# Kernel optimization log

Measured on AMD Instinct MI355X. Metric: run time of the kernel, lower is better.

## Reference

```python
import jax, jax.numpy as jnp
import numpy as np

N_NODES = 100000
N_EDGES = 1600000
DIM = 128
HEADS = 8
PHC = DIM // HEADS  # per-head channels = 16


def setup_inputs() -> dict:
    key = jax.random.key(0)
    k1, k2, k3, k4, k5 = jax.random.split(key, 5)
    nodes = jax.random.normal(k1, (N_NODES, DIM), dtype=jnp.float32)
    senders = jax.random.randint(k2, (N_EDGES,), 0, N_NODES, dtype=jnp.int32)
    receivers = jax.random.randint(k3, (N_EDGES,), 0, N_NODES, dtype=jnp.int32)
    # VarianceScaling(fan_avg, uniform) ~ limit = sqrt(3/fan_avg)
    lim_w = np.sqrt(3.0 / DIM)
    W = jax.random.uniform(k4, (DIM, DIM), minval=-lim_w, maxval=lim_w, dtype=jnp.float32)
    b = jnp.zeros((DIM,), dtype=jnp.float32)
    lim_a = np.sqrt(3.0 * 2.0 / (2 * PHC + 1))
    attn_w = jax.random.uniform(k5, (2 * PHC, 1), minval=-lim_a, maxval=lim_a, dtype=jnp.float32)
    attn_b = jnp.zeros((1,), dtype=jnp.float32)
    return {"nodes": nodes, "senders": senders, "receivers": receivers,
            "W": W, "b": b, "attn_w": attn_w, "attn_b": attn_b}


def reference(nodes, senders, receivers, W, b, attn_w, attn_b):
    n = nodes.shape[0]
    # linear transform + split heads: [N, H, PHC]
    nt = (nodes @ W + b).reshape(n, HEADS, PHC)
    sent = nt[senders]      # [E, H, PHC] gather
    recv = nt[receivers]    # [E, H, PHC] gather
    # attention logits: Linear(1) over leaky_relu(concat(q,k)) -> [E, H, 1]
    qk = jax.nn.leaky_relu(jnp.concatenate([sent, recv], axis=-1), negative_slope=0.2)
    logits = qk @ attn_w + attn_b  # [E, H, 1]
    # segment softmax over edges grouped by receiver node
    seg_max = jax.ops.segment_max(logits, receivers, num_segments=n)  # [N, H, 1]
    exp = jnp.exp(logits - seg_max[receivers])
    denom = jax.ops.segment_sum(exp, receivers, num_segments=n)  # [N, H, 1]
    alpha = exp / denom[receivers]
    # weighted scatter-sum of sender features
    out = jax.ops.segment_sum(sent * alpha, receivers, num_segments=n)  # [N, H, PHC]
    return out.reshape(n, -1)  # concat=True -> [N, DIM]
```

## Files before the change

### kernel.cpp

```cpp
#include <hip/hip_runtime.h>

#define DIM 128
#define HEADS 8
#define PHC 16

#define BSHIFT 6
#define BNODES 64
#define CAP 1408
#define NBMAX 1600

typedef __bf16 bf16x4 __attribute__((ext_vector_type(4)));
typedef __bf16 bf16x8 __attribute__((ext_vector_type(8)));
typedef float  f32x4  __attribute__((ext_vector_type(4)));

__device__ inline unsigned short f2bf(float x) {
  unsigned int u = __float_as_uint(x);
  unsigned int r = (u + 0x7FFF + ((u >> 16) & 1)) >> 16;
  return (unsigned short)r;
}

#define GROWS 64

__global__ __launch_bounds__(256, 3) void k_gemm(
    const float* __restrict__ A, const float* __restrict__ W,
    const float* __restrict__ bias, const float* __restrict__ attn_w,
    unsigned int* __restrict__ nt_bf, float* __restrict__ s_exp,
    int* __restrict__ gCursor, int NB, int n) {
  __shared__ __align__(16) float smemF[GROWS * DIM];
  __bf16* Ah = (__bf16*)smemF;
  __bf16* Al = Ah + GROWS * DIM;
  const int t    = threadIdx.x;
  const int row0 = blockIdx.x * GROWS;
  const int lane = t & 63;
  const int w    = t >> 6;
  const int lg   = lane >> 4;
  const int ln   = lane & 15;

  if (blockIdx.x == 0)
    for (int i = t; i < NB; i += 256) gCursor[i] = 0;

  float4 av[8];
  {
    const float4* A4 = (const float4*)(A + (size_t)row0 * DIM);
    const int lim = min(GROWS, n - row0) * (DIM / 4);
#pragma unroll
    for (int j = 0; j < 8; ++j) {
      int i = t + j * 256;
      av[j] = (i < lim) ? A4[i] : make_float4(0.f, 0.f, 0.f, 0.f);
    }
  }

  bf16x8 Bh[4][2], Bl[4][2];
  {
    const int wc = (w << 5) + ln;
#pragma unroll
    for (int kt = 0; kt < 4; ++kt)
#pragma unroll
      for (int ct = 0; ct < 2; ++ct)
#pragma unroll
        for (int e = 0; e < 8; ++e) {
          int k = (kt << 5) + ((e >> 2) << 4) + (lg << 2) + (e & 3);
          float wv = W[k * DIM + wc + (ct << 4)];
          __bf16 h = (__bf16)wv;
          Bh[kt][ct][e] = h;
          Bl[kt][ct][e] = (__bf16)(wv - (float)h);
        }
  }

#pragma unroll
  for (int j = 0; j < 8; ++j) {
    int i = t + j * 256;
    int r = i >> 5, c4 = i & 31;
    int ei = (r << 7) + ((c4 << 2) ^ ((r & 7) << 3));
    float x0 = av[j].x, x1 = av[j].y, x2 = av[j].z, x3 = av[j].w;
    __bf16 h0 = (__bf16)x0, h1 = (__bf16)x1, h2 = (__bf16)x2, h3 = (__bf16)x3;
    bf16x4 hv = {h0, h1, h2, h3};
    bf16x4 lv = {(__bf16)(x0 - (float)h0), (__bf16)(x1 - (float)h1),
                 (__bf16)(x2 - (float)h2), (__bf16)(x3 - (float)h3)};
    *(bf16x4*)(Ah + ei) = hv;
    *(bf16x4*)(Al + ei) = lv;
  }

  f32x4 acc[4][2];
  {
    const float b0 = bias[(w << 5) + ln];
    const float b1 = bias[(w << 5) + 16 + ln];
#pragma unroll
    for (int rt = 0; rt < 4; ++rt) {
      acc[rt][0] = (f32x4){b0, b0, b0, b0};
      acc[rt][1] = (f32x4){b1, b1, b1, b1};
    }
  }
  __syncthreads();

#pragma unroll
  for (int kt = 0; kt < 4; ++kt) {
    bf16x8 ah[4], al[4];
#pragma unroll
    for (int rt = 0; rt < 4; ++rt) {
      int m    = (rt << 4) + ln;
      int base = m << 7;
      int sw   = (m & 7) << 3;
      int k0   = (kt << 5) + (lg << 2);
      bf16x4 u0 = *(const bf16x4*)(Ah + base + (k0 ^ sw));
      bf16x4 u1 = *(const bf16x4*)(Ah + base + ((k0 + 16) ^ sw));
      bf16x4 v0 = *(const bf16x4*)(Al + base + (k0 ^ sw));
      bf16x4 v1 = *(const bf16x4*)(Al + base + ((k0 + 16) ^ sw));
      ah[rt] = __builtin_shufflevector(u0, u1, 0, 1, 2, 3, 4, 5, 6, 7);
      al[rt] = __builtin_shufflevector(v0, v1, 0, 1, 2, 3, 4, 5, 6, 7);
    }
#pragma unroll
    for (int rt = 0; rt < 4; ++rt)
#pragma unroll
      for (int ct = 0; ct < 2; ++ct) {
        acc[rt][ct] = __builtin_amdgcn_mfma_f32_16x16x32_bf16(
            ah[rt], Bh[kt][ct], acc[rt][ct], 0, 0, 0);
        acc[rt][ct] = __builtin_amdgcn_mfma_f32_16x16x32_bf16(
            ah[rt], Bl[kt][ct], acc[rt][ct], 0, 0, 0);
        acc[rt][ct] = __builtin_amdgcn_mfma_f32_16x16x32_bf16(
            al[rt], Bh[kt][ct], acc[rt][ct], 0, 0, 0);
      }
  }

  __syncthreads();

#pragma unroll
  for (int rt = 0; rt < 4; ++rt)
#pragma unroll
    for (int ct = 0; ct < 2; ++ct) {
      int colx = ((w << 5) + (ct << 4) + ln) ^ ((lg & 1) << 4);
#pragma unroll
      for (int r = 0; r < 4; ++r) {
        int rowl = (rt << 4) + (lg << 2) + r;
        smemF[(rowl << 7) + colx] = acc[rt][ct][r];
      }
    }

  {
    const float aw = attn_w[ln];
#pragma unroll
    for (int rt = 0; rt < 4; ++rt)
#pragma unroll
      for (int ct = 0; ct < 2; ++ct) {
        const int head = (w << 1) + ct;
#pragma unroll
        for (int r = 0; r < 4; ++r) {
          float v = acc[rt][ct][r];
          float p = (v > 0.f ? v : 0.2f * v) * aw;
          p += __shfl_xor(p, 1);
          p += __shfl_xor(p, 2);
          p += __shfl_xor(p, 4);
          p += __shfl_xor(p, 8);
          if (ln == 0) {
            int row = row0 + (rt << 4) + (lg << 2) + r;
            if (row < n) s_exp[row * HEADS + head] = __expf(p);
          }
        }
      }
  }
  __syncthreads();

  {
    const int nrow = min(GROWS, n - row0);
#pragma unroll
    for (int j = 0; j < 8; ++j) {
      int i = t + j * 256;
      int r = i >> 5, c4 = i & 31;
      if (r < nrow) {
        int c4s = c4 ^ (((r >> 2) & 1) << 2);
        f32x4 v = *(const f32x4*)(smemF + (r << 7) + (c4s << 2));
        unsigned int lo = (unsigned int)f2bf(v[0]) | ((unsigned int)f2bf(v[1]) << 16);
        unsigned int hi = (unsigned int)f2bf(v[2]) | ((unsigned int)f2bf(v[3]) << 16);
        ((uint2*)nt_bf)[(size_t)(row0 + r) * 32 + c4] = make_uint2(lo, hi);
      }
    }
  }
}

__global__ __launch_bounds__(256) void k_scatterpairs(
    const int* __restrict__ send, const int* __restrict__ recv,
    int* __restrict__ gCursor, unsigned int* __restrict__ pairs,
    int E, int NB) {
  __shared__ int cnt[NBMAX];
  __shared__ int cur[NBMAX];
  const int t = threadIdx.x;
  for (int i = t; i < NB; i += 256) cnt[i] = 0;
  __syncthreads();
  const int e0 = blockIdx.x * 8192;
  const int e1 = min(e0 + 8192, E);
  for (int i = e0 + t; i < e1; i += 256)
    atomicAdd(&cnt[recv[i] >> BSHIFT], 1);
  __syncthreads();
  for (int i = t; i < NB; i += 256) {
    int c = cnt[i];
    cur[i] = i * CAP + (c ? atomicAdd(&gCursor[i], c) : 0);
  }
  __syncthreads();
  for (int i = e0 + t; i < e1; i += 256) {
    int r = recv[i];
    int b = r >> BSHIFT;
    int p = atomicAdd(&cur[b], 1);
    if (p - b * CAP < CAP)
      pairs[p] = (unsigned int)send[i] | ((unsigned int)(r & (BNODES - 1)) << 17);
  }
}

__global__ __launch_bounds__(256) void k_aggbuild(
    const unsigned int* __restrict__ pairs, const int* __restrict__ gCursor,
    const unsigned int* __restrict__ nt_bf, const float* __restrict__ s_exp,
    float* __restrict__ out, int n) {
  __shared__ unsigned int buf[CAP];
  __shared__ int csr_l[CAP];
  __shared__ int hist[BNODES], offl[BNODES], curl[BNODES];
  const int b = blockIdx.x;
  const int t = threadIdx.x;
  const int base = b * CAP;
  const int bsize = min(gCursor[b], CAP);

  for (int i = t; i < bsize; i += 256) buf[i] = pairs[base + i];
  if (t < BNODES) hist[t] = 0;
  __syncthreads();
  for (int i = t; i < bsize; i += 256)
    atomicAdd(&hist[(buf[i] >> 17) & (BNODES - 1)], 1);
  __syncthreads();
  if (t < 64) {
    int v = hist[t];
    int x = v;
#pragma unroll
    for (int off = 1; off < 64; off <<= 1) {
      int y = __shfl_up(x, off);
      if (t >= off) x += y;
    }
    offl[t] = x - v;
    curl[t] = x - v;
  }
  __syncthreads();
  for (int i = t; i < bsize; i += 256) {
    unsigned int v = buf[i];
    int p = atomicAdd(&curl[(v >> 17) & (BNODES - 1)], 1);
    csr_l[p] = (int)(v & 0x1FFFF);
  }
  __syncthreads();

  const int wv = t >> 6;
  const int lane = t & 63;
  const int half = lane >> 5;
  const int l32 = lane & 31;
  const int head = l32 >> 2;
  const uint2* nt2 = (const uint2*)nt_bf;

#pragma unroll 1
  for (int pi = 0; pi < 8; ++pi) {
    const int nl = wv * 16 + pi * 2 + half;
    const int node = (b << BSHIFT) + nl;
    const int deg = hist[nl];
    const int eoff = offl[nl];
    float4 acc = make_float4(0.f, 0.f, 0.f, 0.f);
    float den = 0.f;
    for (int j = 0; j < deg; j += 2) {
      int s0 = csr_l[eoff + j];
      bool ok1 = (j + 1) < deg;
      int s1 = csr_l[ok1 ? (eoff + j + 1) : eoff];
      float w0 = s_exp[s0 * HEADS + head];
      float w1 = ok1 ? s_exp[s1 * HEADS + head] : 0.f;
      uint2 q0 = nt2[(size_t)s0 * 32 + l32];
      uint2 q1 = nt2[(size_t)s1 * 32 + l32];
      den += w0 + w1;
      acc.x = fmaf(w0, __uint_as_float(q0.x << 16),
              fmaf(w1, __uint_as_float(q1.x << 16), acc.x));
      acc.y = fmaf(w0, __uint_as_float(q0.x & 0xFFFF0000u),
              fmaf(w1, __uint_as_float(q1.x & 0xFFFF0000u), acc.y));
      acc.z = fmaf(w0, __uint_as_float(q0.y << 16),
              fmaf(w1, __uint_as_float(q1.y << 16), acc.z));
      acc.w = fmaf(w0, __uint_as_float(q0.y & 0xFFFF0000u),
              fmaf(w1, __uint_as_float(q1.y & 0xFFFF0000u), acc.w));
    }
    if (node < n) {
      const float inv = (deg > 0) ? 1.0f / den : 0.f;
      ((float4*)out)[(size_t)node * 32 + l32] =
          make_float4(acc.x * inv, acc.y * inv, acc.z * inv, acc.w * inv);
    }
  }
}

extern "C" void kernel_launch(void* const* d_in, const int* in_sizes, int n_in,
                              void* d_out, int out_size, void* d_ws, size_t ws_size,
                              hipStream_t stream) {
  const float* nodes   = (const float*)d_in[0];
  const int*   senders = (const int*)d_in[1];
  const int*   recvs   = (const int*)d_in[2];
  const float* W       = (const float*)d_in[3];
  const float* bias    = (const float*)d_in[4];
  const float* attn_w  = (const float*)d_in[5];

  const int n = in_sizes[0] / DIM;
  const int E = in_sizes[1];
  const int NB = (n + BNODES - 1) >> BSHIFT;

  char* w = (char*)d_ws;
  auto align256 = [](size_t x) { return (x + 255) & ~(size_t)255; };
  size_t off = 0;
  unsigned int* nt_bf = (unsigned int*)(w + off); off += align256((size_t)n * DIM * 2);
  float* s_exp   = (float*)(w + off); off += align256((size_t)n * HEADS * 4);
  unsigned int* pairs = (unsigned int*)(w + off); off += align256((size_t)NB * CAP * 4);
  int* gCursor   = (int*)(w + off);   off += align256((size_t)NB * 4);
  (void)ws_size;

  k_gemm<<<(n + GROWS - 1) / GROWS, 256, 0, stream>>>(nodes, W, bias, attn_w,
                                                      nt_bf, s_exp, gCursor, NB, n);
  const int nb1 = (E + 8191) / 8192;
  k_scatterpairs<<<nb1, 256, 0, stream>>>(senders, recvs, gCursor, pairs, E, NB);
  k_aggbuild<<<NB, 256, 0, stream>>>(pairs, gCursor, nt_bf, s_exp,
                                     (float*)d_out, n);
}
```

Before: 274.7 us.

## Pre-split W into bf16 hi/lo fragments, widen LDS reads and aggregation loads

Adds a small kernel that converts W into MFMA-ready bf16 hi/lo fragment arrays once, so each GEMM block loads fragments per k-tile with vector loads instead of gathering and splitting 128 scalars per thread. This also lowers register pressure. The A tile in LDS is re-swizzled at 16-byte units so each fragment is a single bf16x8 read. The aggregation kernel now processes four nodes per wave with 16 lanes each, using 16-byte loads and a 4-way unrolled edge loop to get more memory-level parallelism, at the cost of one extra launch and more live registers.

Measured after the change: 268.2 us. 1.02x faster.

```diff
diff --git a/kernel.cpp b/kernel.cpp
--- a/kernel.cpp
+++ b/kernel.cpp
@@ -19,13 +19,35 @@
   return (unsigned short)r;
 }
 
+__global__ __launch_bounds__(256) void k_prepw(
+    const float* __restrict__ W, __bf16* __restrict__ Wh,
+    __bf16* __restrict__ Wl) {
+  const int tuple = blockIdx.x * 256 + threadIdx.x;
+  const int ln = tuple & 15;
+  const int lg = (tuple >> 4) & 3;
+  const int cg = (tuple >> 6) & 7;
+  const int kt = tuple >> 9;
+  const int col = (cg << 4) + ln;
+  bf16x8 h, l;
+#pragma unroll
+  for (int e = 0; e < 8; ++e) {
+    int k = (kt << 5) + ((e >> 2) << 4) + (lg << 2) + (e & 3);
+    float wv = W[k * DIM + col];
+    __bf16 hh = (__bf16)wv;
+    h[e] = hh;
+    l[e] = (__bf16)(wv - (float)hh);
+  }
+  *(bf16x8*)(Wh + tuple * 8) = h;
+  *(bf16x8*)(Wl + tuple * 8) = l;
+}
+
 #define GROWS 64
 
 __global__ __launch_bounds__(256, 3) void k_gemm(
-    const float* __restrict__ A, const float* __restrict__ W,
-    const float* __restrict__ bias, const float* __restrict__ attn_w,
-    unsigned int* __restrict__ nt_bf, float* __restrict__ s_exp,
-    int* __restrict__ gCursor, int NB, int n) {
+    const float* __restrict__ A, const __bf16* __restrict__ Wh,
+    const __bf16* __restrict__ Wl, const float* __restrict__ bias,
+    const float* __restrict__ attn_w, unsigned int* __restrict__ nt_bf,
+    float* __restrict__ s_exp, int* __restrict__ gCursor, int NB, int n) {
   __shared__ __align__(16) float smemF[GROWS * DIM];
   __bf16* Ah = (__bf16*)smemF;
   __bf16* Al = Ah + GROWS * DIM;
@@ -50,28 +72,13 @@
     }
   }
 
-  bf16x8 Bh[4][2], Bl[4][2];
-  {
-    const int wc = (w << 5) + ln;
-#pragma unroll
-    for (int kt = 0; kt < 4; ++kt)
-#pragma unroll
-      for (int ct = 0; ct < 2; ++ct)
-#pragma unroll
-        for (int e = 0; e < 8; ++e) {
-          int k = (kt << 5) + ((e >> 2) << 4) + (lg << 2) + (e & 3);
-          float wv = W[k * DIM + wc + (ct << 4)];
-          __bf16 h = (__bf16)wv;
-          Bh[kt][ct][e] = h;
-          Bl[kt][ct][e] = (__bf16)(wv - (float)h);
-        }
-  }
-
 #pragma unroll
   for (int j = 0; j < 8; ++j) {
     int i = t + j * 256;
     int r = i >> 5, c4 = i & 31;
-    int ei = (r << 7) + ((c4 << 2) ^ ((r & 7) << 3));
+    int ktc = c4 >> 3, lgc = c4 & 3, ehi = (c4 >> 2) & 1;
+    int unit = (r << 4) + (((ktc << 2) + lgc) ^ (r & 15));
+    int ei = (unit << 3) + (ehi << 2);
     float x0 = av[j].x, x1 = av[j].y, x2 = av[j].z, x3 = av[j].w;
     __bf16 h0 = (__bf16)x0, h1 = (__bf16)x1, h2 = (__bf16)x2, h3 = (__bf16)x3;
     bf16x4 hv = {h0, h1, h2, h3};
@@ -93,33 +100,35 @@
   }
   __syncthreads();
 
+  const int cg0 = w << 1;
 #pragma unroll
   for (int kt = 0; kt < 4; ++kt) {
+    bf16x8 Bh0, Bl0, Bh1, Bl1;
+    {
+      int i0 = ((((kt << 3) + cg0) << 2) + lg) * 16 + ln;
+      int i1 = ((((kt << 3) + cg0 + 1) << 2) + lg) * 16 + ln;
+      Bh0 = *(const bf16x8*)(Wh + (i0 << 3));
+      Bl0 = *(const bf16x8*)(Wl + (i0 << 3));
+      Bh1 = *(const bf16x8*)(Wh + (i1 << 3));
+      Bl1 = *(const bf16x8*)(Wl + (i1 << 3));
+    }
     bf16x8 ah[4], al[4];
 #pragma unroll
     for (int rt = 0; rt < 4; ++rt) {
-      int m    = (rt << 4) + ln;
-      int base = m << 7;
-      int sw   = (m & 7) << 3;
-      int k0   = (kt << 5) + (lg << 2);
-      bf16x4 u0 = *(const bf16x4*)(Ah + base + (k0 ^ sw));
-      bf16x4 u1 = *(const bf16x4*)(Ah + base + ((k0 + 16) ^ sw));
-      bf16x4 v0 = *(const bf16x4*)(Al + base + (k0 ^ sw));
-      bf16x4 v1 = *(const bf16x4*)(Al + base + ((k0 + 16) ^ sw));
-      ah[rt] = __builtin_shufflevector(u0, u1, 0, 1, 2, 3, 4, 5, 6, 7);
-      al[rt] = __builtin_shufflevector(v0, v1, 0, 1, 2, 3, 4, 5, 6, 7);
-    }
-#pragma unroll
-    for (int rt = 0; rt < 4; ++rt)
-#pragma unroll
-      for (int ct = 0; ct < 2; ++ct) {
-        acc[rt][ct] = __builtin_amdgcn_mfma_f32_16x16x32_bf16(
-            ah[rt], Bh[kt][ct], acc[rt][ct], 0, 0, 0);
-        acc[rt][ct] = __builtin_amdgcn_mfma_f32_16x16x32_bf16(
-            ah[rt], Bl[kt][ct], acc[rt][ct], 0, 0, 0);
-        acc[rt][ct] = __builtin_amdgcn_mfma_f32_16x16x32_bf16(
-            al[rt], Bh[kt][ct], acc[rt][ct], 0, 0, 0);
-      }
+      int m = (rt << 4) + ln;
+      int u = (m << 4) + (((kt << 2) + lg) ^ (m & 15));
+      ah[rt] = *(const bf16x8*)(Ah + (u << 3));
+      al[rt] = *(const bf16x8*)(Al + (u << 3));
+    }
+#pragma unroll
+    for (int rt = 0; rt < 4; ++rt) {
+      acc[rt][0] = __builtin_amdgcn_mfma_f32_16x16x32_bf16(ah[rt], Bh0, acc[rt][0], 0, 0, 0);
+      acc[rt][0] = __builtin_amdgcn_mfma_f32_16x16x32_bf16(ah[rt], Bl0, acc[rt][0], 0, 0, 0);
+      acc[rt][0] = __builtin_amdgcn_mfma_f32_16x16x32_bf16(al[rt], Bh0, acc[rt][0], 0, 0, 0);
+      acc[rt][1] = __builtin_amdgcn_mfma_f32_16x16x32_bf16(ah[rt], Bh1, acc[rt][1], 0, 0, 0);
+      acc[rt][1] = __builtin_amdgcn_mfma_f32_16x16x32_bf16(ah[rt], Bl1, acc[rt][1], 0, 0, 0);
+      acc[rt][1] = __builtin_amdgcn_mfma_f32_16x16x32_bf16(al[rt], Bh1, acc[rt][1], 0, 0, 0);
+    }
   }
 
   __syncthreads();
@@ -205,6 +214,17 @@
   }
 }
 
+__device__ inline void acc8(float wgt, uint4 qv, float4& a0, float4& a1) {
+  a0.x = fmaf(wgt, __uint_as_float(qv.x << 16), a0.x);
+  a0.y = fmaf(wgt, __uint_as_float(qv.x & 0xFFFF0000u), a0.y);
+  a0.z = fmaf(wgt, __uint_as_float(qv.y << 16), a0.z);
+  a0.w = fmaf(wgt, __uint_as_float(qv.y & 0xFFFF0000u), a0.w);
+  a1.x = fmaf(wgt, __uint_as_float(qv.z << 16), a1.x);
+  a1.y = fmaf(wgt, __uint_as_float(qv.z & 0xFFFF0000u), a1.y);
+  a1.z = fmaf(wgt, __uint_as_float(qv.w << 16), a1.z);
+  a1.w = fmaf(wgt, __uint_as_float(qv.w & 0xFFFF0000u), a1.w);
+}
+
 __global__ __launch_bounds__(256) void k_aggbuild(
     const unsigned int* __restrict__ pairs, const int* __restrict__ gCursor,
     const unsigned int* __restrict__ nt_bf, const float* __restrict__ s_exp,
@@ -242,43 +262,47 @@
   }
   __syncthreads();
 
-  const int wv = t >> 6;
+  const int wv   = t >> 6;
   const int lane = t & 63;
-  const int half = lane >> 5;
-  const int l32 = lane & 31;
-  const int head = l32 >> 2;
-  const uint2* nt2 = (const uint2*)nt_bf;
+  const int q    = lane >> 4;
+  const int l16  = lane & 15;
+  const int head = l16 >> 1;
+  const uint4* nt4 = (const uint4*)nt_bf;
 
 #pragma unroll 1
-  for (int pi = 0; pi < 8; ++pi) {
-    const int nl = wv * 16 + pi * 2 + half;
+  for (int pi = 0; pi < 4; ++pi) {
+    const int nl = wv * 16 + pi * 4 + q;
     const int node = (b << BSHIFT) + nl;
     const int deg = hist[nl];
     const int eoff = offl[nl];
-    float4 acc = make_float4(0.f, 0.f, 0.f, 0.f);
+    float4 a0 = make_float4(0.f, 0.f, 0.f, 0.f);
+    float4 a1 = make_float4(0.f, 0.f, 0.f, 0.f);
     float den = 0.f;
-    for (int j = 0; j < deg; j += 2) {
+    for (int j = 0; j < deg; j += 4) {
+      bool ok1 = (j + 1) < deg, ok2 = (j + 2) < deg, ok3 = (j + 3) < deg;
       int s0 = csr_l[eoff + j];
-      bool ok1 = (j + 1) < deg;
       int s1 = csr_l[ok1 ? (eoff + j + 1) : eoff];
+      int s2 = csr_l[ok2 ? (eoff + j + 2) : eoff];
+      int s3 = csr_l[ok3 ? (eoff + j + 3) : eoff];
       float w0 = s_exp[s0 * HEADS + head];
       float w1 = ok1 ? s_exp[s1 * HEADS + head] : 0.f;
-      uint2 q0 = nt2[(size_t)s0 * 32 + l32];
-      uint2 q1 = nt2[(size_t)s1 * 32 + l32];
-      den += w0 + w1;
-      acc.x = fmaf(w0, __uint_as_float(q0.x << 16),
-              fmaf(w1, __uint_as_float(q1.x << 16), acc.x));
-      acc.y = fmaf(w0, __uint_as_float(q0.x & 0xFFFF0000u),
-              fmaf(w1, __uint_as_float(q1.x & 0xFFFF0000u), acc.y));
-      acc.z = fmaf(w0, __uint_as_float(q0.y << 16),
-              fmaf(w1, __uint_as_float(q1.y << 16), acc.z));
-      acc.w = fmaf(w0, __uint_as_float(q0.y & 0xFFFF0000u),
-              fmaf(w1, __uint_as_float(q1.y & 0xFFFF0000u), acc.w));
+      float w2 = ok2 ? s_exp[s2 * HEADS + head] : 0.f;
+      float w3 = ok3 ? s_exp[s3 * HEADS + head] : 0.f;
+      uint4 q0 = nt4[(size_t)s0 * 16 + l16];
+      uint4 q1 = nt4[(size_t)s1 * 16 + l16];
+      uint4 q2 = nt4[(size_t)s2 * 16 + l16];
+      uint4 q3 = nt4[(size_t)s3 * 16 + l16];
+      den += (w0 + w1) + (w2 + w3);
+      acc8(w0, q0, a0, a1);
+      acc8(w1, q1, a0, a1);
+      acc8(w2, q2, a0, a1);
+      acc8(w3, q3, a0, a1);
     }
     if (node < n) {
       const float inv = (deg > 0) ? 1.0f / den : 0.f;
-      ((float4*)out)[(size_t)node * 32 + l32] =
-          make_float4(acc.x * inv, acc.y * inv, acc.z * inv, acc.w * inv);
+      float4* op = (float4*)out + (size_t)node * 32 + l16 * 2;
+      op[0] = make_float4(a0.x * inv, a0.y * inv, a0.z * inv, a0.w * inv);
+      op[1] = make_float4(a1.x * inv, a1.y * inv, a1.z * inv, a1.w * inv);
     }
   }
 }
@@ -304,9 +328,12 @@
   float* s_exp   = (float*)(w + off); off += align256((size_t)n * HEADS * 4);
   unsigned int* pairs = (unsigned int*)(w + off); off += align256((size_t)NB * CAP * 4);
   int* gCursor   = (int*)(w + off);   off += align256((size_t)NB * 4);
+  __bf16* Wh     = (__bf16*)(w + off); off += align256((size_t)2048 * 8 * 2);
+  __bf16* Wl     = (__bf16*)(w + off); off += align256((size_t)2048 * 8 * 2);
   (void)ws_size;
 
-  k_gemm<<<(n + GROWS - 1) / GROWS, 256, 0, stream>>>(nodes, W, bias, attn_w,
+  k_prepw<<<8, 256, 0, stream>>>(W, Wh, Wl);
+  k_gemm<<<(n + GROWS - 1) / GROWS, 256, 0, stream>>>(nodes, Wh, Wl, bias, attn_w,
                                                       nt_bf, s_exp, gCursor, NB, n);
   const int nb1 = (E + 8191) / 8192;
   k_scatterpairs<<<nb1, 256, 0, stream>>>(senders, recvs, gCursor, pairs, E, NB);
```
